# Optimization experiments

Hardware: AMD Instinct MI355X
Metric: run time of the kernel (lower is better)

Reference implementation:

```python
import jax, jax.numpy as jnp
import numpy as np

B = 65536
R = 160            # radial_len (capped at MAX_RADIAL_LEN)
EDGE_SINK_WIDTH = 8


def setup_inputs() -> dict:
    key = jax.random.key(0)
    k1, k2 = jax.random.split(key)
    return {
        "history": jax.random.uniform(k1, (B, R, 3), dtype=jnp.float32),
        "color_rgb": jax.random.uniform(k2, (B, 3), dtype=jnp.float32),
        "offset_per_frame_60hz": jnp.float32(1.3),
        "persistence_per_frame_60hz": jnp.float32(0.92),
        "diffusion01": jnp.float32(0.5),
        "dt_seconds": jnp.float32(1.0 / 60.0),
        "amount01": jnp.float32(0.8),
        "spread01": jnp.float32(0.4),
    }


def _forward(history, color_rgb, offset, persistence, diffusion01, dt_seconds, amount01, spread01):
    dt = jnp.clip(dt_seconds, 0.0, 0.05)
    dt_scale = dt * 60.0
    dt_offset = offset * dt_scale
    dt_persist = persistence ** dt_scale

    # ---- inject at centre: 5-bin spread kernel, then clamp to [0,1] ----
    amount = jnp.clip(amount01, 0.0, 1.0)
    spread = jnp.clip(spread01, 0.0, 1.0)
    energy = color_rgb * amount                      # [B,3]
    tight = 1.0 - spread
    w = jnp.stack([0.5 + 0.4 * tight,
                   0.2 * spread + 0.05,
                   0.12 * spread,
                   0.06 * spread,
                   0.02 * spread])                   # [5]
    h = history.at[:, :5, :].add(energy[:, None, :] * w[None, :, None])
    h = jnp.clip(h, 0.0, 1.0)

    # ---- semi-Lagrangian push advection (vectorized scatter-add) ----
    i = jnp.arange(R, dtype=h.dtype)                 # source bin positions
    new_pos = i + dt_offset
    valid = (new_pos >= 0.0) & (new_pos < R - 1)     # bins outside are dropped
    left = jnp.clip(jnp.floor(new_pos).astype(jnp.int32), 0, R - 2)
    frac = new_pos - left.astype(h.dtype)
    wl = jnp.where(valid, (1.0 - frac) * dt_persist, 0.0)  # [R]
    wr = jnp.where(valid, frac * dt_persist, 0.0)
    work = jnp.zeros_like(h)
    work = work.at[:, left, :].add(h * wl[None, :, None])
    work = work.at[:, left + 1, :].add(h * wr[None, :, None])
    h = work

    # ---- diffusion: [k, 1-2k, k] stencil with ZERO boundary taps ----
    k = 0.15 * diffusion01
    c = 1.0 - 2.0 * k
    padded = jnp.pad(h, ((0, 0), (1, 1), (0, 0)))    # zero pad matches torch boundary
    h = c * h + k * padded[:, :-2, :] + k * padded[:, 2:, :]

    # ---- quadratic edge sink over last EDGE_SINK_WIDTH bins ----
    idx = jnp.arange(R)
    t = (R - 1 - idx).astype(h.dtype) / float(EDGE_SINK_WIDTH)
    fade = jnp.where(idx >= R - EDGE_SINK_WIDTH, t * t, jnp.ones((), h.dtype))
    h = h * fade[None, :, None]
    return h


def reference(history, color_rgb, offset_per_frame_60hz, persistence_per_frame_60hz,
              diffusion01, dt_seconds, amount01, spread01):
    return _forward(history, color_rgb, offset_per_frame_60hz,
                    persistence_per_frame_60hz, diffusion01, dt_seconds,
                    amount01, spread01)
```

## Files before the change

kernel.cpp:

```cpp
#include <hip/hip_runtime.h>
#include <math.h>

#define RBINS 160
#define BROWS 65536
#define ROWELEMS 480
#define NELEM (BROWS * ROWELEMS)
#define TILE_ROWS 8
#define TILE_F (TILE_ROWS * ROWELEMS)
#define TILE_F4 (TILE_F / 4)
#define NTHREADS 320
#define NBLOCKS (BROWS / TILE_ROWS)

__device__ __forceinline__ float clamp01(float x) {
    return __builtin_amdgcn_fmed3f(x, 0.0f, 1.0f);
}

template<int P>
__device__ __forceinline__ void compute_store(
    const float4* __restrict__ tile4, const float* __restrict__ gp,
    float* __restrict__ outp, int w4base)
{
    float w[32];
    #pragma unroll
    for (int q = 0; q < 8; ++q) {
        int idx = w4base + q;
        idx = min(max(idx, 0), TILE_F4 - 1);
        float4 v = tile4[idx];
        w[4*q+0] = v.x; w[4*q+1] = v.y; w[4*q+2] = v.z; w[4*q+3] = v.w;
    }
    #pragma unroll
    for (int u = 0; u < 32; ++u) w[u] = clamp01(w[u]);

    float G[24];
    #pragma unroll
    for (int q = 0; q < 24; ++q) G[q] = gp[q];

    float r[12];
    #pragma unroll
    for (int m = 0; m < 12; ++m) {
        const int gb = (m / 3) * 6;
        float acc = G[gb+0] * w[P+m+0];
        acc += G[gb+1] * w[P+m+3];
        acc += G[gb+2] * w[P+m+6];
        acc += G[gb+3] * w[P+m+9];
        acc += G[gb+4] * w[P+m+12];
        acc += G[gb+5] * w[P+m+15];
        r[m] = acc;
    }
    float4* dst = (float4*)outp;
    dst[0] = make_float4(r[0], r[1], r[2],  r[3]);
    dst[1] = make_float4(r[4], r[5], r[6],  r[7]);
    dst[2] = make_float4(r[8], r[9], r[10], r[11]);
}

__global__ __launch_bounds__(NTHREADS, 4) void beat_kernel(
    const float* __restrict__ hist,
    const float* __restrict__ color,
    const float* __restrict__ p_offset,
    const float* __restrict__ p_persist,
    const float* __restrict__ p_diff,
    const float* __restrict__ p_dt,
    const float* __restrict__ p_amount,
    const float* __restrict__ p_spread,
    float* __restrict__ out)
{
    __shared__ float tile[TILE_F];
    __shared__ float g_lds[RBINS * 6];
    __shared__ float aw_lds[8];
    __shared__ int   d_lds;

    const int tid = threadIdx.x;

    if (tid < RBINS) {
        const float offs = *p_offset;
        const float pers = *p_persist;
        const float diff = *p_diff;
        const float dts  = *p_dt;

        const float dt       = fminf(fmaxf(dts, 0.0f), 0.05f);
        const float dt_scale = dt * 60.0f;
        const float s        = offs * dt_scale;
        const float dt_pers  = powf(pers, dt_scale);
        const int   dfl      = (int)floorf(s);
        const float kk = 0.15f * diff;
        const float cc = 1.0f - 2.0f * kk;

        const int j = tid;
        float fade = 1.0f;
        if (j >= RBINS - 8) {
            const float tt = (float)(RBINS - 1 - j) * 0.125f;
            fade = tt * tt;
        }
        const int i0 = j - dfl - 3;
        #pragma unroll
        for (int t = 0; t < 6; ++t) {
            float coef = 0.0f;
            const int i = i0 + t;
            if (i >= 0 && i < RBINS) {
                const float np_ = (float)i + s;
                if (np_ >= 0.0f && np_ < (float)(RBINS - 1)) {
                    int left = (int)floorf(np_);
                    left = min(max(left, 0), RBINS - 2);
                    const float frac = np_ - (float)left;
                    const float wl = (1.0f - frac) * dt_pers;
                    const float wr = frac * dt_pers;
                    const int dl = j - left;
                    const int dr = j - (left + 1);
                    const float cl = (dl == 0) ? cc : ((dl == 1 || dl == -1) ? kk : 0.0f);
                    const float cr = (dr == 0) ? cc : ((dr == 1 || dr == -1) ? kk : 0.0f);
                    coef = wl * cl + wr * cr;
                }
            }
            g_lds[j * 6 + t] = coef * fade;
        }
        if (tid == 0) {
            const float am = fminf(fmaxf(*p_amount, 0.0f), 1.0f);
            const float sp = fminf(fmaxf(*p_spread, 0.0f), 1.0f);
            const float tight = 1.0f - sp;
            aw_lds[0] = am * (0.5f + 0.4f * tight);
            aw_lds[1] = am * (0.2f * sp + 0.05f);
            aw_lds[2] = am * (0.12f * sp);
            aw_lds[3] = am * (0.06f * sp);
            aw_lds[4] = am * (0.02f * sp);
            d_lds = dfl;
        }
    }

    {
        const float4* src = (const float4*)hist;
        float4* t4 = (float4*)tile;
        const int base4 = blockIdx.x * TILE_F4;
        #pragma unroll
        for (int q = 0; q < TILE_F4 / NTHREADS; ++q) {
            const int idx = q * NTHREADS + tid;
            t4[idx] = src[base4 + idx];
        }
    }
    __syncthreads();

    if (tid < TILE_ROWS * 15) {
        const int r = tid / 15;
        const int e = tid - r * 15;
        const int i = e / 3;
        const int ch = e - 3 * i;
        const int b = blockIdx.x * TILE_ROWS + r;
        tile[r * ROWELEMS + e] += color[b * 3 + ch] * aw_lds[i];
    }
    __syncthreads();

    const int r  = tid / 40;
    const int c  = tid - r * 40;
    const int e0 = c * 12;
    const int j0 = c * 4;

    const int dfl = d_lds;
    const int S   = (dfl + 3) * 3;
    const int p   = (-S) & 3;
    const int a0  = e0 - S - p;
    const int w4base = r * (ROWELEMS / 4) + (a0 >> 2);

    const float* gp = &g_lds[j0 * 6];
    float* outp = out + (blockIdx.x * TILE_ROWS + r) * ROWELEMS + e0;
    const float4* tile4 = (const float4*)tile;

    switch (p) {
        case 0:  compute_store<0>(tile4, gp, outp, w4base); break;
        case 1:  compute_store<1>(tile4, gp, outp, w4base); break;
        case 2:  compute_store<2>(tile4, gp, outp, w4base); break;
        default: compute_store<3>(tile4, gp, outp, w4base); break;
    }
}

extern "C" void kernel_launch(void* const* d_in, const int* in_sizes, int n_in,
                              void* d_out, int out_size, void* d_ws, size_t ws_size,
                              hipStream_t stream) {
    const float* hist      = (const float*)d_in[0];
    const float* color     = (const float*)d_in[1];
    const float* p_offset  = (const float*)d_in[2];
    const float* p_persist = (const float*)d_in[3];
    const float* p_diff    = (const float*)d_in[4];
    const float* p_dt      = (const float*)d_in[5];
    const float* p_amount  = (const float*)d_in[6];
    const float* p_spread  = (const float*)d_in[7];
    float* outp = (float*)d_out;

    beat_kernel<<<dim3(NBLOCKS), dim3(NTHREADS), 0, stream>>>(
        hist, color, p_offset, p_persist, p_diff, p_dt, p_amount, p_spread, outp);
}
```

Measured before the change: 236.1 us.

## Drop LDS tiling; compute stencil directly from global loads with uniform 4-tap weights

Removes the shared-memory tile, the per-bin coefficient table and both block barriers. Each thread now loads its own overlapping window of the row straight from global memory. The 6-tap per-bin coefficients become four uniform taps computed in registers, with validity masking done by bin range and the fade applied only to the last tasks of each row. Centre injection is folded into the register window. The goal is to cut LDS traffic and sync overhead and raise occupancy. The cost is redundant overlapping global loads, which the cache must absorb, and __powf replacing powf.

```diff
diff --git a/kernel.cpp b/kernel.cpp
--- a/kernel.cpp
+++ b/kernel.cpp
@@ -4,56 +4,46 @@
 #define RBINS 160
 #define BROWS 65536
 #define ROWELEMS 480
-#define NELEM (BROWS * ROWELEMS)
-#define TILE_ROWS 8
-#define TILE_F (TILE_ROWS * ROWELEMS)
-#define TILE_F4 (TILE_F / 4)
-#define NTHREADS 320
-#define NBLOCKS (BROWS / TILE_ROWS)
+#define ROWF4 (ROWELEMS / 4)
+#define TASKS_PER_ROW 40
+#define NTHREADS 256
+#define TOTAL_TASKS (BROWS * TASKS_PER_ROW)
+#define NBLOCKS (TOTAL_TASKS / NTHREADS)
 
 __device__ __forceinline__ float clamp01(float x) {
     return __builtin_amdgcn_fmed3f(x, 0.0f, 1.0f);
 }
 
 template<int P>
-__device__ __forceinline__ void compute_store(
-    const float4* __restrict__ tile4, const float* __restrict__ gp,
-    float* __restrict__ outp, int w4base)
+__device__ __forceinline__ void stencil_store(
+    const float* __restrict__ w,
+    float u1, float u2, float u3, float u4,
+    float4* __restrict__ dst, bool dofade, int j0)
 {
-    float w[32];
-    #pragma unroll
-    for (int q = 0; q < 8; ++q) {
-        int idx = w4base + q;
-        idx = min(max(idx, 0), TILE_F4 - 1);
-        float4 v = tile4[idx];
-        w[4*q+0] = v.x; w[4*q+1] = v.y; w[4*q+2] = v.z; w[4*q+3] = v.w;
-    }
-    #pragma unroll
-    for (int u = 0; u < 32; ++u) w[u] = clamp01(w[u]);
-
-    float G[24];
-    #pragma unroll
-    for (int q = 0; q < 24; ++q) G[q] = gp[q];
-
     float r[12];
     #pragma unroll
     for (int m = 0; m < 12; ++m) {
-        const int gb = (m / 3) * 6;
-        float acc = G[gb+0] * w[P+m+0];
-        acc += G[gb+1] * w[P+m+3];
-        acc += G[gb+2] * w[P+m+6];
-        acc += G[gb+3] * w[P+m+9];
-        acc += G[gb+4] * w[P+m+12];
-        acc += G[gb+5] * w[P+m+15];
+        float acc = u1 * w[P + m];
+        acc = fmaf(u2, w[P + m + 3], acc);
+        acc = fmaf(u3, w[P + m + 6], acc);
+        acc = fmaf(u4, w[P + m + 9], acc);
         r[m] = acc;
     }
-    float4* dst = (float4*)outp;
+    if (dofade) {
+        #pragma unroll
+        for (int mb = 0; mb < 4; ++mb) {
+            const int j = j0 + mb;
+            const float t = (float)(RBINS - 1 - j) * 0.125f;
+            const float ff = (j >= RBINS - 8) ? t * t : 1.0f;
+            r[3*mb+0] *= ff; r[3*mb+1] *= ff; r[3*mb+2] *= ff;
+        }
+    }
     dst[0] = make_float4(r[0], r[1], r[2],  r[3]);
     dst[1] = make_float4(r[4], r[5], r[6],  r[7]);
     dst[2] = make_float4(r[8], r[9], r[10], r[11]);
 }
 
-__global__ __launch_bounds__(NTHREADS, 4) void beat_kernel(
+__global__ __launch_bounds__(NTHREADS, 6) void beat_kernel(
     const float* __restrict__ hist,
     const float* __restrict__ color,
     const float* __restrict__ p_offset,
@@ -64,110 +54,91 @@
     const float* __restrict__ p_spread,
     float* __restrict__ out)
 {
-    __shared__ float tile[TILE_F];
-    __shared__ float g_lds[RBINS * 6];
-    __shared__ float aw_lds[8];
-    __shared__ int   d_lds;
+    const int task = blockIdx.x * NTHREADS + threadIdx.x;
+    const int b = task / TASKS_PER_ROW;
+    const int c = task - b * TASKS_PER_ROW;
 
-    const int tid = threadIdx.x;
+    const float offs = *p_offset;
+    const float pers = *p_persist;
+    const float diff = *p_diff;
+    const float dts  = *p_dt;
 
-    if (tid < RBINS) {
-        const float offs = *p_offset;
-        const float pers = *p_persist;
-        const float diff = *p_diff;
-        const float dts  = *p_dt;
+    const float dt       = fminf(fmaxf(dts, 0.0f), 0.05f);
+    const float dt_scale = dt * 60.0f;
+    const float s        = offs * dt_scale;
+    const float dt_pers  = __powf(pers, dt_scale);
+    const int   dfl      = (int)floorf(s);
+    const float frac     = s - (float)dfl;
+    const float kk = 0.15f * diff;
+    const float cc = 1.0f - 2.0f * kk;
+    const float wl = (1.0f - frac) * dt_pers;
+    const float wr = frac * dt_pers;
+    const float u1 = wr * kk;
+    const float u2 = fmaf(wl, kk, wr * cc);
+    const float u3 = fmaf(wl, cc, wr * kk);
+    const float u4 = wl * kk;
 
-        const float dt       = fminf(fmaxf(dts, 0.0f), 0.05f);
-        const float dt_scale = dt * 60.0f;
-        const float s        = offs * dt_scale;
-        const float dt_pers  = powf(pers, dt_scale);
-        const int   dfl      = (int)floorf(s);
-        const float kk = 0.15f * diff;
-        const float cc = 1.0f - 2.0f * kk;
+    const int ilo = max(0, (int)ceilf(-s));
+    const int ihi = min(RBINS - 1, (int)ceilf((float)(RBINS - 1) - s) - 1);
+    const int flo = 3 * ilo;
+    const int fhi = 3 * ihi + 3;
 
-        const int j = tid;
-        float fade = 1.0f;
-        if (j >= RBINS - 8) {
-            const float tt = (float)(RBINS - 1 - j) * 0.125f;
-            fade = tt * tt;
-        }
-        const int i0 = j - dfl - 3;
+    const int e0 = c * 12;
+    const int A  = e0 - 6 - 3 * dfl;
+    const int p  = A & 3;
+    const int a0 = A - p;
+
+    const float4* src4 = (const float4*)hist + (size_t)b * ROWF4;
+    float w[24];
+    #pragma unroll
+    for (int q = 0; q < 6; ++q) {
+        int idx = (a0 >> 2) + q;
+        idx = min(max(idx, 0), ROWF4 - 1);
+        const float4 v = src4[idx];
+        w[4*q+0] = v.x; w[4*q+1] = v.y; w[4*q+2] = v.z; w[4*q+3] = v.w;
+    }
+
+    if (a0 < 15) {
+        const float am = fminf(fmaxf(*p_amount, 0.0f), 1.0f);
+        const float sp = fminf(fmaxf(*p_spread, 0.0f), 1.0f);
+        const float tight = 1.0f - sp;
+        const float aw0 = am * fmaf(0.4f, tight, 0.5f);
+        const float aw1 = am * fmaf(0.2f, sp, 0.05f);
+        const float aw2 = am * (0.12f * sp);
+        const float aw3 = am * (0.06f * sp);
+        const float aw4 = am * (0.02f * sp);
+        const float c0 = color[3*b+0];
+        const float c1 = color[3*b+1];
+        const float c2 = color[3*b+2];
         #pragma unroll
-        for (int t = 0; t < 6; ++t) {
-            float coef = 0.0f;
-            const int i = i0 + t;
-            if (i >= 0 && i < RBINS) {
-                const float np_ = (float)i + s;
-                if (np_ >= 0.0f && np_ < (float)(RBINS - 1)) {
-                    int left = (int)floorf(np_);
-                    left = min(max(left, 0), RBINS - 2);
-                    const float frac = np_ - (float)left;
-                    const float wl = (1.0f - frac) * dt_pers;
-                    const float wr = frac * dt_pers;
-                    const int dl = j - left;
-                    const int dr = j - (left + 1);
-                    const float cl = (dl == 0) ? cc : ((dl == 1 || dl == -1) ? kk : 0.0f);
-                    const float cr = (dr == 0) ? cc : ((dr == 1 || dr == -1) ? kk : 0.0f);
-                    coef = wl * cl + wr * cr;
-                }
+        for (int u = 0; u < 24; ++u) {
+            const int f = a0 + u;
+            if ((unsigned)f < 15u) {
+                const int bin = f / 3;
+                const int ch  = f - 3 * bin;
+                const float cv = (ch == 0) ? c0 : (ch == 1) ? c1 : c2;
+                const float av = (bin == 0) ? aw0 : (bin == 1) ? aw1 :
+                                 (bin == 2) ? aw2 : (bin == 3) ? aw3 : aw4;
+                w[u] += cv * av;
             }
-            g_lds[j * 6 + t] = coef * fade;
-        }
-        if (tid == 0) {
-            const float am = fminf(fmaxf(*p_amount, 0.0f), 1.0f);
-            const float sp = fminf(fmaxf(*p_spread, 0.0f), 1.0f);
-            const float tight = 1.0f - sp;
-            aw_lds[0] = am * (0.5f + 0.4f * tight);
-            aw_lds[1] = am * (0.2f * sp + 0.05f);
-            aw_lds[2] = am * (0.12f * sp);
-            aw_lds[3] = am * (0.06f * sp);
-            aw_lds[4] = am * (0.02f * sp);
-            d_lds = dfl;
         }
     }
 
-    {
-        const float4* src = (const float4*)hist;
-        float4* t4 = (float4*)tile;
-        const int base4 = blockIdx.x * TILE_F4;
-        #pragma unroll
-        for (int q = 0; q < TILE_F4 / NTHREADS; ++q) {
-            const int idx = q * NTHREADS + tid;
-            t4[idx] = src[base4 + idx];
-        }
+    #pragma unroll
+    for (int u = 0; u < 24; ++u) {
+        const int f = a0 + u;
+        const bool m = (f >= flo) && (f < fhi);
+        w[u] = m ? clamp01(w[u]) : 0.0f;
     }
-    __syncthreads();
 
-    if (tid < TILE_ROWS * 15) {
-        const int r = tid / 15;
-        const int e = tid - r * 15;
-        const int i = e / 3;
-        const int ch = e - 3 * i;
-        const int b = blockIdx.x * TILE_ROWS + r;
-        tile[r * ROWELEMS + e] += color[b * 3 + ch] * aw_lds[i];
-    }
-    __syncthreads();
-
-    const int r  = tid / 40;
-    const int c  = tid - r * 40;
-    const int e0 = c * 12;
-    const int j0 = c * 4;
-
-    const int dfl = d_lds;
-    const int S   = (dfl + 3) * 3;
-    const int p   = (-S) & 3;
-    const int a0  = e0 - S - p;
-    const int w4base = r * (ROWELEMS / 4) + (a0 >> 2);
-
-    const float* gp = &g_lds[j0 * 6];
-    float* outp = out + (blockIdx.x * TILE_ROWS + r) * ROWELEMS + e0;
-    const float4* tile4 = (const float4*)tile;
-
+    float4* dst = (float4*)(out + (size_t)b * ROWELEMS + e0);
+    const bool dofade = (c >= TASKS_PER_ROW - 2);
+    const int j0 = 4 * c;
     switch (p) {
-        case 0:  compute_store<0>(tile4, gp, outp, w4base); break;
-        case 1:  compute_store<1>(tile4, gp, outp, w4base); break;
-        case 2:  compute_store<2>(tile4, gp, outp, w4base); break;
-        default: compute_store<3>(tile4, gp, outp, w4base); break;
+        case 0:  stencil_store<0>(w, u1, u2, u3, u4, dst, dofade, j0); break;
+        case 1:  stencil_store<1>(w, u1, u2, u3, u4, dst, dofade, j0); break;
+        case 2:  stencil_store<2>(w, u1, u2, u3, u4, dst, dofade, j0); break;
+        default: stencil_store<3>(w, u1, u2, u3, u4, dst, dofade, j0); break;
     }
 }
 
```

Result: faster. 230.8 us (-2.2%).
